# Kernel optimization log

Hardware: AMD Instinct MI355X
Metric: run time of the kernel (lower is better)

## Reference

```python
import jax, jax.numpy as jnp
import numpy as np

# Model dims
E, K, D, F = 8, 2, 1024, 2048   # num_experts, top_k, d_model, d_ff
B, S = 2, 1024                  # batch, seq -> T = 2048 tokens


def setup_inputs() -> dict:
    key = jax.random.key(0)
    k1, k2, k3, k4 = jax.random.split(key, 4)
    hidden = jax.random.normal(k1, (B, S, D), dtype=jnp.float32)
    gate_logits = jax.random.normal(k2, (B * S, E), dtype=jnp.float32)
    # Expert FFN params: expert_e(x) = silu(x @ W1[e]) @ W2[e]
    W1 = jax.random.normal(k3, (E, D, F), dtype=jnp.float32) * 0.02
    W2 = jax.random.normal(k4, (E, F, D), dtype=jnp.float32) * 0.02
    return {"hidden": hidden, "gate_logits": gate_logits, "W1": W1, "W2": W2}


def reference(hidden, gate_logits, W1, W2):
    b, s, d = hidden.shape
    x = hidden.reshape(-1, d)                                  # [T, D]
    # Router: softmax -> top-k -> renormalize (gate_logits path of forward)
    probs = jax.nn.softmax(gate_logits, axis=-1)               # [T, E]
    topk_w, topk_idx = jax.lax.top_k(probs, K)                 # [T, K]
    topk_w = topk_w / jnp.sum(topk_w, axis=-1, keepdims=True)
    # Combine weights as a dense [T, E] map (top_k indices are distinct)
    tok_w = jnp.sum(jax.nn.one_hot(topk_idx, E, dtype=topk_w.dtype)
                    * topk_w[..., None], axis=1)               # [T, E]
    # Grouped expert FFN, expressed densely over the expert axis; the
    # combine weights zero out non-selected experts, so the math equals the
    # original gather -> per-expert GEMM -> weighted scatter-combine.
    h = jax.nn.silu(jnp.einsum('td,edf->tef', x, W1))          # [T, E, F]
    y = jnp.einsum('tef,efd->ted', h, W2)                      # [T, E, D]
    out = jnp.einsum('te,ted->td', tok_w, y)                   # [T, D]
    return out.reshape(b, s, d)
```

## Files before the change

### kernel.cpp

```cpp
#include <hip/hip_runtime.h>
#include <hip/hip_bf16.h>

#define E_N 8
#define D_DIM 1024
#define F_DIM 2048
#define T_N 2048
#define NSLOT 4096

typedef unsigned short u16;
typedef unsigned int u32;
typedef unsigned long long u64;
typedef float floatx4 __attribute__((ext_vector_type(4)));
typedef short bf16x8v __attribute__((ext_vector_type(8)));

__device__ __forceinline__ u16 f2bf(float f) {
    union { float f; u32 u; } v; v.f = f;
    u32 r = v.u + 0x7FFFu + ((v.u >> 16) & 1u);
    return (u16)(r >> 16);
}

__device__ __forceinline__ void gll16(const void* g, void* l) {
    __builtin_amdgcn_global_load_lds((const __attribute__((address_space(1))) void*)g,
                                     (__attribute__((address_space(3))) void*)l, 16, 0, 0);
}

__global__ __launch_bounds__(256) void router_kernel(const float* __restrict__ gl,
                                                     int4* __restrict__ tok_meta,
                                                     float* __restrict__ tok_w0,
                                                     int* __restrict__ bcnt) {
    __shared__ int scnt[E_N];
    const int tid = threadIdx.x, b = blockIdx.x;
    if (tid < E_N) scnt[tid] = 0;
    __syncthreads();
    const int t = b * 256 + tid;
    const float4* gp = (const float4*)(gl + (size_t)t * E_N);
    const float4 x0 = gp[0], x1 = gp[1];
    float l[E_N] = {x0.x, x0.y, x0.z, x0.w, x1.x, x1.y, x1.z, x1.w};
    int e0 = 0; float m0 = l[0];
#pragma unroll
    for (int e = 1; e < E_N; ++e) if (l[e] > m0) { m0 = l[e]; e0 = e; }
    int e1 = -1; float m1 = -1e30f;
#pragma unroll
    for (int e = 0; e < E_N; ++e) if (e != e0 && l[e] > m1) { m1 = l[e]; e1 = e; }
    const float p = __expf(m1 - m0);
    const float w0 = 1.0f / (1.0f + p);
    const int r0 = atomicAdd(&scnt[e0], 1);
    const int r1 = atomicAdd(&scnt[e1], 1);
    tok_meta[t] = make_int4(e0, e1, r0, r1);
    tok_w0[t] = w0;
    __syncthreads();
    if (tid < E_N) bcnt[b * E_N + tid] = scnt[tid];
}

__device__ __forceinline__ void cvt_pair(const float* __restrict__ src, u16* __restrict__ dst,
                                         int R, int C, int tr, int tcp, int e, char* LT) {
    const int r0 = tr << 6, c0 = tcp << 7;
    const int t = threadIdx.x;
    const int rowq = t >> 4, col4 = t & 15;
    const float* sp = src + (size_t)e * R * C + (size_t)(r0 + rowq * 4) * C + c0 + col4 * 4;
    float4 v0[4], v1[4];
#pragma unroll
    for (int i = 0; i < 4; ++i) v0[i] = *(const float4*)(sp + (size_t)i * C);
#pragma unroll
    for (int i = 0; i < 4; ++i) v1[i] = *(const float4*)(sp + (size_t)i * C + 64);
    u16* dp = dst + (size_t)e * R * C;

    const float* f0 = (const float*)v0;
#pragma unroll
    for (int j = 0; j < 4; ++j) {
        const int c = col4 * 4 + j;
        u64 pk = (u64)f2bf(f0[0 * 4 + j]) | ((u64)f2bf(f0[1 * 4 + j]) << 16)
               | ((u64)f2bf(f0[2 * 4 + j]) << 32) | ((u64)f2bf(f0[3 * 4 + j]) << 48);
        *(u64*)(LT + c * 144 + ((rowq ^ col4) << 3)) = pk;
    }
    __syncthreads();
#pragma unroll
    for (int i = 0; i < 2; ++i) {
        const int id = i * 256 + t;
        const int c = id >> 3, seg = id & 7;
        const int x = (c >> 2) & 15;
        u64 q[2];
        q[0] = *(const u64*)(LT + c * 144 + (((2 * seg) ^ x) << 3));
        q[1] = *(const u64*)(LT + c * 144 + (((2 * seg + 1) ^ x) << 3));
        *(uint4*)(dp + (size_t)(c0 + c) * R + r0 + seg * 8) = *(const uint4*)q;
    }
    const float* f1 = (const float*)v1;
#pragma unroll
    for (int j = 0; j < 4; ++j) {
        const int c = col4 * 4 + j;
        u64 pk = (u64)f2bf(f1[0 * 4 + j]) | ((u64)f2bf(f1[1 * 4 + j]) << 16)
               | ((u64)f2bf(f1[2 * 4 + j]) << 32) | ((u64)f2bf(f1[3 * 4 + j]) << 48);
        *(u64*)(LT + 9216 + c * 144 + ((rowq ^ col4) << 3)) = pk;
    }
    __syncthreads();
#pragma unroll
    for (int i = 0; i < 2; ++i) {
        const int id = i * 256 + t;
        const int c = id >> 3, seg = id & 7;
        const int x = (c >> 2) & 15;
        u64 q[2];
        q[0] = *(const u64*)(LT + 9216 + c * 144 + (((2 * seg) ^ x) << 3));
        q[1] = *(const u64*)(LT + 9216 + c * 144 + (((2 * seg + 1) ^ x) << 3));
        *(uint4*)(dp + (size_t)(c0 + 64 + c) * R + r0 + seg * 8) = *(const uint4*)q;
    }
}

__global__ __launch_bounds__(256) void prep_kernel(
        const float* __restrict__ W1, const float* __restrict__ W2,
        const float* __restrict__ X, float* __restrict__ out,
        const int4* __restrict__ tok_meta, const float* __restrict__ tok_w0,
        const int* __restrict__ bcnt,
        int* __restrict__ cnt, int* __restrict__ basep,
        int* __restrict__ slot_tok, float* __restrict__ slot_w,
        u16* __restrict__ W1T, u16* __restrict__ W2T, u16* __restrict__ Xg) {
    __shared__ __align__(16) char LT[18432];
    __shared__ int sb[64];
    const int b = blockIdx.x;
    const int tid = threadIdx.x;
    if (b < 2048) {
        const int e = b >> 8, p = b & 255;
        cvt_pair(W1, W1T, D_DIM, F_DIM, p >> 4, p & 15, e, LT);
    } else if (b < 4096) {
        const int b2 = b - 2048;
        const int e = b2 >> 8, p = b2 & 255;
        cvt_pair(W2, W2T, F_DIM, D_DIM, p >> 3, p & 7, e, LT);
    } else if (b < 4608) {
        const int g = b - 4096;
        if (tid < 64) sb[tid] = bcnt[tid];
        __syncthreads();
        int cntE[E_N], baseE[E_N];
        {
            int s = 0;
#pragma unroll
            for (int e = 0; e < E_N; ++e) {
                int c = 0;
#pragma unroll
                for (int k = 0; k < 8; ++k) c += sb[k * E_N + e];
                cntE[e] = c; baseE[e] = s; s += c;
            }
        }
        const int t = g * 4 + (tid >> 6), lane = tid & 63;
        const int4 mt = tok_meta[t];
        const float w0 = tok_w0[t];
        const int bt = t >> 8;
        int o0 = baseE[mt.x], o1 = baseE[mt.y];
        for (int k = 0; k < bt; ++k) { o0 += sb[k * E_N + mt.x]; o1 += sb[k * E_N + mt.y]; }
        const int s0 = o0 + mt.z, s1 = o1 + mt.w;
        const float* xp = X + (size_t)t * D_DIM + lane * 4;
        u16* g0 = Xg + (size_t)s0 * D_DIM + lane * 4;
        u16* g1 = Xg + (size_t)s1 * D_DIM + lane * 4;
#pragma unroll
        for (int p = 0; p < 4; ++p) {
            const float4 v = *(const float4*)(xp + p * 256);
            union { u16 o[4]; uint2 q; } u;
            u.o[0] = f2bf(v.x); u.o[1] = f2bf(v.y); u.o[2] = f2bf(v.z); u.o[3] = f2bf(v.w);
            *(uint2*)(g0 + p * 256) = u.q;
            *(uint2*)(g1 + p * 256) = u.q;
        }
        if (lane == 0) {
            slot_tok[s0] = t; slot_tok[s1] = t;
            slot_w[s0] = w0; slot_w[s1] = 1.0f - w0;
        }
        if (g == 0 && tid < E_N) { cnt[tid] = cntE[tid]; basep[tid] = baseE[tid]; }
    } else {
        const int z = b - 4608;
        float4 zq = {0.f, 0.f, 0.f, 0.f};
        float* op = out + (size_t)z * 2048 + tid * 8;
        *(float4*)op = zq;
        *(float4*)(op + 4) = zq;
    }
}

template<bool G1>
__global__ __launch_bounds__(256) void moe_gemm_kernel(
        const u16* __restrict__ A, const u16* __restrict__ B,
        const int* __restrict__ cnt, const int* __restrict__ basep,
        const int* __restrict__ slot_tok, const float* __restrict__ slot_w,
        u16* __restrict__ hout, float* __restrict__ out) {
    constexpr int KA = G1 ? D_DIM : F_DIM;
    constexpr int KB = KA;
    constexpr int KIT = 16;
    const int e  = G1 ? blockIdx.z : (blockIdx.z >> 1);
    const int kh = G1 ? 0 : (blockIdx.z & 1);
    const int mt = blockIdx.y;
    const int nt = blockIdx.x;
    const int cnt_e = cnt[e];
    if (mt * 128 >= cnt_e) return;
    const int m0 = basep[e] + mt * 128;
    const int vm = cnt_e - mt * 128;

    __shared__ __align__(16) u16 Alds[8192];
    __shared__ __align__(16) u16 Blds[8192];

    const int tid = threadIdx.x;
    const int wid = tid >> 6, lane = tid & 63;
    const int l3 = lane >> 3, l7 = lane & 7;
    const int stgRow = wid * 8 + l3;
    const int stgCol = ((l7 ^ l3) << 3);

    const u16* aS = A + (size_t)(m0 + stgRow) * KA + kh * (F_DIM / 2) + stgCol;
    const u16* bS = B + (size_t)e * ((size_t)D_DIM * F_DIM)
                      + (size_t)(nt * 128 + stgRow) * KB + kh * (F_DIM / 2) + stgCol;

    const int wm = (wid >> 1) * 64, wn = (wid & 1) * 64;
    const int lr = lane & 15, lq = lane >> 4;
    const int aoff = (wm + lr) * 64;
    const int boff = (wn + lr) * 64;
    const int sw0 = ((lq)     ^ l7) << 3;
    const int sw1 = ((lq + 4) ^ l7) << 3;

    floatx4 acc[4][4];
    const floatx4 zero = {0.f, 0.f, 0.f, 0.f};
#pragma unroll
    for (int i = 0; i < 4; ++i)
#pragma unroll
        for (int j = 0; j < 4; ++j) acc[i][j] = zero;

    for (int kt = 0; kt < KIT; ++kt) {
#pragma unroll
        for (int c = 0; c < 4; ++c) {
            gll16(aS + (size_t)(c * 32) * KA, &Alds[c * 2048 + wid * 512]);
            gll16(bS + (size_t)(c * 32) * KB, &Blds[c * 2048 + wid * 512]);
        }
        aS += 64; bS += 64;
        __syncthreads();
#pragma unroll
        for (int ks = 0; ks < 2; ++ks) {
            const int sw = ks ? sw1 : sw0;
            bf16x8v af[4], bfv[4];
#pragma unroll
            for (int mi = 0; mi < 4; ++mi) af[mi]  = *(const bf16x8v*)&Alds[aoff + mi * 1024 + sw];
#pragma unroll
            for (int ni = 0; ni < 4; ++ni) bfv[ni] = *(const bf16x8v*)&Blds[boff + ni * 1024 + sw];
#pragma unroll
            for (int mi = 0; mi < 4; ++mi)
#pragma unroll
                for (int ni = 0; ni < 4; ++ni)
                    acc[mi][ni] = __builtin_amdgcn_mfma_f32_16x16x32_bf16(af[mi], bfv[ni], acc[mi][ni], 0, 0, 0);
        }
        __syncthreads();
    }

    if constexpr (G1) {
#pragma unroll
        for (int mi = 0; mi < 4; ++mi)
#pragma unroll
            for (int r = 0; r < 4; ++r) {
                const int rl = wm + mi * 16 + lq * 4 + r;
                if (rl < vm) {
                    const float w = slot_w[m0 + rl];
                    u16* hp = hout + (size_t)(m0 + rl) * F_DIM + nt * 128 + wn + lr;
#pragma unroll
                    for (int ni = 0; ni < 4; ++ni) {
                        const float v = acc[mi][ni][r];
                        hp[ni * 16] = f2bf(w * v / (1.0f + __expf(-v)));
                    }
                }
            }
    } else {
#pragma unroll
        for (int mi = 0; mi < 4; ++mi)
#pragma unroll
            for (int r = 0; r < 4; ++r) {
                const int rl = wm + mi * 16 + lq * 4 + r;
                if (rl < vm) {
                    const int tok = slot_tok[m0 + rl];
                    float* op = out + (size_t)tok * D_DIM + nt * 128 + wn + lr;
#pragma unroll
                    for (int ni = 0; ni < 4; ++ni) atomicAdd(&op[ni * 16], acc[mi][ni][r]);
                }
            }
    }
}

extern "C" void kernel_launch(void* const* d_in, const int* in_sizes, int n_in,
                              void* d_out, int out_size, void* d_ws, size_t ws_size,
                              hipStream_t stream) {
    const float* hidden = (const float*)d_in[0];
    const float* gl     = (const float*)d_in[1];
    const float* W1     = (const float*)d_in[2];
    const float* W2     = (const float*)d_in[3];
    float* out = (float*)d_out;

    char* ws = (char*)d_ws;
    int*   cnt      = (int*)(ws + 0);
    int*   basep    = (int*)(ws + 64);
    int*   bcnt     = (int*)(ws + 128);
    int4*  tok_meta = (int4*)(ws + 512);
    float* tok_w0   = (float*)(ws + 512 + 32768);
    int*   slot_tok = (int*)(ws + 512 + 40960);
    float* slot_w   = (float*)(ws + 512 + 57344);

    const size_t META    = 131072;
    const size_t HBYTES  = (size_t)(NSLOT + 128) * F_DIM * 2;
    const size_t W1BYTES = (size_t)E_N * D_DIM * F_DIM * 2;
    const size_t XBYTES  = (size_t)(NSLOT + 128) * D_DIM * 2;
    u16* h   = (u16*)(ws + META);
    u16* W1T = (u16*)(ws + META + HBYTES);
    u16* Xg  = (u16*)(ws + META + HBYTES + W1BYTES);
    u16* W2T = (u16*)(ws + META + HBYTES + W1BYTES + XBYTES);

    router_kernel<<<8, 256, 0, stream>>>(gl, tok_meta, tok_w0, bcnt);
    prep_kernel<<<5632, 256, 0, stream>>>(W1, W2, hidden, out, tok_meta, tok_w0, bcnt,
                                          cnt, basep, slot_tok, slot_w, W1T, W2T, Xg);
    moe_gemm_kernel<true><<<dim3(F_DIM / 128, 16, E_N), 256, 0, stream>>>(
        Xg, W1T, cnt, basep, slot_tok, slot_w, h, nullptr);
    moe_gemm_kernel<false><<<dim3(D_DIM / 128, 16, E_N * 2), 256, 0, stream>>>(
        h, W2T, cnt, basep, slot_tok, slot_w, nullptr, out);
}
```

Baseline: 258.9 us.

## Fuse fp32-to-bf16 weight and activation conversion into MoE GEMM tile loads

Removes the separate prep pass that transposed and converted W1/W2 to bf16 and gathered X into a bf16 buffer. The GEMM kernels now read fp32 weights and gathered token rows directly, convert them with v_cvt_pk_bf16_f32 and store them into swizzled LDS. The second GEMM drops its K-split. The aim is to avoid writing and re-reading bf16 copies of the weights, but every expert tile now re-reads and re-converts fp32 weights, using synchronous scalar-strided loads instead of async global-to-LDS loads, which gives up load/compute overlap.

```diff
diff --git a/kernel.cpp b/kernel.cpp
--- a/kernel.cpp
+++ b/kernel.cpp
@@ -13,10 +13,10 @@
 typedef float floatx4 __attribute__((ext_vector_type(4)));
 typedef short bf16x8v __attribute__((ext_vector_type(8)));
 
-__device__ __forceinline__ u16 f2bf(float f) {
-    union { float f; u32 u; } v; v.f = f;
-    u32 r = v.u + 0x7FFFu + ((v.u >> 16) & 1u);
-    return (u16)(r >> 16);
+__device__ __forceinline__ u32 cvtpk(float a, float b) {
+    u32 r;
+    asm("v_cvt_pk_bf16_f32 %0, %1, %2" : "=v"(r) : "v"(a), "v"(b));
+    return r;
 }
 
 __device__ __forceinline__ void gll16(const void* g, void* l) {
@@ -52,138 +52,58 @@
     if (tid < E_N) bcnt[b * E_N + tid] = scnt[tid];
 }
 
-__device__ __forceinline__ void cvt_pair(const float* __restrict__ src, u16* __restrict__ dst,
-                                         int R, int C, int tr, int tcp, int e, char* LT) {
-    const int r0 = tr << 6, c0 = tcp << 7;
-    const int t = threadIdx.x;
-    const int rowq = t >> 4, col4 = t & 15;
-    const float* sp = src + (size_t)e * R * C + (size_t)(r0 + rowq * 4) * C + c0 + col4 * 4;
-    float4 v0[4], v1[4];
-#pragma unroll
-    for (int i = 0; i < 4; ++i) v0[i] = *(const float4*)(sp + (size_t)i * C);
-#pragma unroll
-    for (int i = 0; i < 4; ++i) v1[i] = *(const float4*)(sp + (size_t)i * C + 64);
-    u16* dp = dst + (size_t)e * R * C;
-
-    const float* f0 = (const float*)v0;
-#pragma unroll
-    for (int j = 0; j < 4; ++j) {
-        const int c = col4 * 4 + j;
-        u64 pk = (u64)f2bf(f0[0 * 4 + j]) | ((u64)f2bf(f0[1 * 4 + j]) << 16)
-               | ((u64)f2bf(f0[2 * 4 + j]) << 32) | ((u64)f2bf(f0[3 * 4 + j]) << 48);
-        *(u64*)(LT + c * 144 + ((rowq ^ col4) << 3)) = pk;
-    }
-    __syncthreads();
-#pragma unroll
-    for (int i = 0; i < 2; ++i) {
-        const int id = i * 256 + t;
-        const int c = id >> 3, seg = id & 7;
-        const int x = (c >> 2) & 15;
-        u64 q[2];
-        q[0] = *(const u64*)(LT + c * 144 + (((2 * seg) ^ x) << 3));
-        q[1] = *(const u64*)(LT + c * 144 + (((2 * seg + 1) ^ x) << 3));
-        *(uint4*)(dp + (size_t)(c0 + c) * R + r0 + seg * 8) = *(const uint4*)q;
-    }
-    const float* f1 = (const float*)v1;
-#pragma unroll
-    for (int j = 0; j < 4; ++j) {
-        const int c = col4 * 4 + j;
-        u64 pk = (u64)f2bf(f1[0 * 4 + j]) | ((u64)f2bf(f1[1 * 4 + j]) << 16)
-               | ((u64)f2bf(f1[2 * 4 + j]) << 32) | ((u64)f2bf(f1[3 * 4 + j]) << 48);
-        *(u64*)(LT + 9216 + c * 144 + ((rowq ^ col4) << 3)) = pk;
-    }
-    __syncthreads();
-#pragma unroll
-    for (int i = 0; i < 2; ++i) {
-        const int id = i * 256 + t;
-        const int c = id >> 3, seg = id & 7;
-        const int x = (c >> 2) & 15;
-        u64 q[2];
-        q[0] = *(const u64*)(LT + 9216 + c * 144 + (((2 * seg) ^ x) << 3));
-        q[1] = *(const u64*)(LT + 9216 + c * 144 + (((2 * seg + 1) ^ x) << 3));
-        *(uint4*)(dp + (size_t)(c0 + 64 + c) * R + r0 + seg * 8) = *(const uint4*)q;
-    }
-}
-
-__global__ __launch_bounds__(256) void prep_kernel(
-        const float* __restrict__ W1, const float* __restrict__ W2,
-        const float* __restrict__ X, float* __restrict__ out,
+__global__ __launch_bounds__(256) void finalize_kernel(
         const int4* __restrict__ tok_meta, const float* __restrict__ tok_w0,
         const int* __restrict__ bcnt,
         int* __restrict__ cnt, int* __restrict__ basep,
         int* __restrict__ slot_tok, float* __restrict__ slot_w,
-        u16* __restrict__ W1T, u16* __restrict__ W2T, u16* __restrict__ Xg) {
-    __shared__ __align__(16) char LT[18432];
-    __shared__ int sb[64];
-    const int b = blockIdx.x;
-    const int tid = threadIdx.x;
-    if (b < 2048) {
-        const int e = b >> 8, p = b & 255;
-        cvt_pair(W1, W1T, D_DIM, F_DIM, p >> 4, p & 15, e, LT);
-    } else if (b < 4096) {
-        const int b2 = b - 2048;
-        const int e = b2 >> 8, p = b2 & 255;
-        cvt_pair(W2, W2T, F_DIM, D_DIM, p >> 3, p & 7, e, LT);
-    } else if (b < 4608) {
-        const int g = b - 4096;
+        float* __restrict__ out) {
+    const int b = blockIdx.x, tid = threadIdx.x;
+    if (b < 8) {
+        __shared__ int sb[64];
         if (tid < 64) sb[tid] = bcnt[tid];
         __syncthreads();
         int cntE[E_N], baseE[E_N];
-        {
-            int s = 0;
-#pragma unroll
-            for (int e = 0; e < E_N; ++e) {
-                int c = 0;
-#pragma unroll
-                for (int k = 0; k < 8; ++k) c += sb[k * E_N + e];
-                cntE[e] = c; baseE[e] = s; s += c;
-            }
-        }
-        const int t = g * 4 + (tid >> 6), lane = tid & 63;
+        int s = 0;
+#pragma unroll
+        for (int e = 0; e < E_N; ++e) {
+            int c = 0;
+#pragma unroll
+            for (int k = 0; k < 8; ++k) c += sb[k * E_N + e];
+            cntE[e] = c; baseE[e] = s; s += c;
+        }
+        const int t = b * 256 + tid;
         const int4 mt = tok_meta[t];
+        int o0 = baseE[mt.x], o1 = baseE[mt.y];
+        for (int k = 0; k < b; ++k) { o0 += sb[k * E_N + mt.x]; o1 += sb[k * E_N + mt.y]; }
+        const int s0 = o0 + mt.z, s1 = o1 + mt.w;
         const float w0 = tok_w0[t];
-        const int bt = t >> 8;
-        int o0 = baseE[mt.x], o1 = baseE[mt.y];
-        for (int k = 0; k < bt; ++k) { o0 += sb[k * E_N + mt.x]; o1 += sb[k * E_N + mt.y]; }
-        const int s0 = o0 + mt.z, s1 = o1 + mt.w;
-        const float* xp = X + (size_t)t * D_DIM + lane * 4;
-        u16* g0 = Xg + (size_t)s0 * D_DIM + lane * 4;
-        u16* g1 = Xg + (size_t)s1 * D_DIM + lane * 4;
-#pragma unroll
-        for (int p = 0; p < 4; ++p) {
-            const float4 v = *(const float4*)(xp + p * 256);
-            union { u16 o[4]; uint2 q; } u;
-            u.o[0] = f2bf(v.x); u.o[1] = f2bf(v.y); u.o[2] = f2bf(v.z); u.o[3] = f2bf(v.w);
-            *(uint2*)(g0 + p * 256) = u.q;
-            *(uint2*)(g1 + p * 256) = u.q;
-        }
-        if (lane == 0) {
-            slot_tok[s0] = t; slot_tok[s1] = t;
-            slot_w[s0] = w0; slot_w[s1] = 1.0f - w0;
-        }
-        if (g == 0 && tid < E_N) { cnt[tid] = cntE[tid]; basep[tid] = baseE[tid]; }
+        slot_tok[s0] = t; slot_tok[s1] = t;
+        slot_w[s0] = w0; slot_w[s1] = 1.0f - w0;
+        if (b == 0 && tid < E_N) { cnt[tid] = cntE[tid]; basep[tid] = baseE[tid]; }
+        if (b == 0) slot_tok[NSLOT + tid] = 0;
     } else {
-        const int z = b - 4608;
-        float4 zq = {0.f, 0.f, 0.f, 0.f};
-        float* op = out + (size_t)z * 2048 + tid * 8;
-        *(float4*)op = zq;
-        *(float4*)(op + 4) = zq;
+        const int z = b - 8;
+        const float4 zq = {0.f, 0.f, 0.f, 0.f};
+        float* op = out + (size_t)z * 4096 + tid * 16;
+        *(float4*)op = zq; *(float4*)(op + 4) = zq;
+        *(float4*)(op + 8) = zq; *(float4*)(op + 12) = zq;
     }
 }
 
 template<bool G1>
-__global__ __launch_bounds__(256) void moe_gemm_kernel(
-        const u16* __restrict__ A, const u16* __restrict__ B,
+__global__ __launch_bounds__(256, 3) void moe_gemm_kernel(
+        const float* __restrict__ Xf, const u16* __restrict__ Ah,
+        const float* __restrict__ Wf,
         const int* __restrict__ cnt, const int* __restrict__ basep,
         const int* __restrict__ slot_tok, const float* __restrict__ slot_w,
         u16* __restrict__ hout, float* __restrict__ out) {
-    constexpr int KA = G1 ? D_DIM : F_DIM;
-    constexpr int KB = KA;
-    constexpr int KIT = 16;
-    const int e  = G1 ? blockIdx.z : (blockIdx.z >> 1);
-    const int kh = G1 ? 0 : (blockIdx.z & 1);
-    const int mt = blockIdx.y;
-    const int nt = blockIdx.x;
+    constexpr int KDIM = G1 ? D_DIM : F_DIM;
+    constexpr int NDIM = G1 ? F_DIM : D_DIM;
+    constexpr int KIT  = KDIM / 64;
+    const int mt = blockIdx.x;
+    const int nt = blockIdx.y;
+    const int e  = blockIdx.z;
     const int cnt_e = cnt[e];
     if (mt * 128 >= cnt_e) return;
     const int m0 = basep[e] + mt * 128;
@@ -194,19 +114,26 @@
 
     const int tid = threadIdx.x;
     const int wid = tid >> 6, lane = tid & 63;
-    const int l3 = lane >> 3, l7 = lane & 7;
-    const int stgRow = wid * 8 + l3;
-    const int stgCol = ((l7 ^ l3) << 3);
-
-    const u16* aS = A + (size_t)(m0 + stgRow) * KA + kh * (F_DIM / 2) + stgCol;
-    const u16* bS = B + (size_t)e * ((size_t)D_DIM * F_DIM)
-                      + (size_t)(nt * 128 + stgRow) * KB + kh * (F_DIM / 2) + stgCol;
+
+    const float* aF = nullptr; const u16* aH = nullptr;
+    const int awm = tid >> 1, awk = (tid & 1) * 4;
+    if constexpr (G1) {
+        const int tok = slot_tok[m0 + awm];
+        aF = Xf + (size_t)tok * D_DIM + (tid & 1) * 32;
+    } else {
+        const int l3 = lane >> 3, l7 = lane & 7;
+        aH = Ah + (size_t)(m0 + wid * 8 + l3) * KDIM + ((l7 ^ l3) << 3);
+    }
+
+    const int n_loc = tid & 127;
+    const int bh = __builtin_amdgcn_readfirstlane(tid >> 7);
+    const float* bBase = Wf + (size_t)e * KDIM * NDIM + (size_t)(bh * 32) * NDIM + nt * 128;
 
     const int wm = (wid >> 1) * 64, wn = (wid & 1) * 64;
-    const int lr = lane & 15, lq = lane >> 4;
+    const int lr = lane & 15, lq = lane >> 4, l7 = lane & 7;
     const int aoff = (wm + lr) * 64;
     const int boff = (wn + lr) * 64;
-    const int sw0 = ((lq)     ^ l7) << 3;
+    const int sw0 = (lq ^ l7) << 3;
     const int sw1 = ((lq + 4) ^ l7) << 3;
 
     floatx4 acc[4][4];
@@ -217,12 +144,45 @@
         for (int j = 0; j < 4; ++j) acc[i][j] = zero;
 
     for (int kt = 0; kt < KIT; ++kt) {
-#pragma unroll
-        for (int c = 0; c < 4; ++c) {
-            gll16(aS + (size_t)(c * 32) * KA, &Alds[c * 2048 + wid * 512]);
-            gll16(bS + (size_t)(c * 32) * KB, &Blds[c * 2048 + wid * 512]);
-        }
-        aS += 64; bS += 64;
+        if constexpr (G1) {
+            float4 av[8];
+#pragma unroll
+            for (int i = 0; i < 8; ++i) av[i] = *(const float4*)(aF + i * 4);
+            aF += 64;
+            const float* f = (const float*)av;
+#pragma unroll
+            for (int c = 0; c < 4; ++c) {
+                const u32 w0 = cvtpk(f[c * 8 + 0], f[c * 8 + 1]);
+                const u32 w1 = cvtpk(f[c * 8 + 2], f[c * 8 + 3]);
+                const u32 w2 = cvtpk(f[c * 8 + 4], f[c * 8 + 5]);
+                const u32 w3 = cvtpk(f[c * 8 + 6], f[c * 8 + 7]);
+                const int s = awk + c;
+                *(uint4*)((char*)Alds + awm * 128 + ((s ^ (awm & 7)) << 4)) =
+                    make_uint4(w0, w1, w2, w3);
+            }
+        } else {
+#pragma unroll
+            for (int c = 0; c < 4; ++c)
+                gll16(aH + (size_t)(c * 32) * KDIM, (char*)Alds + c * 4096 + wid * 1024);
+            aH += 64;
+        }
+        {
+            const size_t krow = (size_t)kt * 64 * NDIM;
+#pragma unroll
+            for (int q = 0; q < 4; ++q) {
+                float v[8];
+#pragma unroll
+                for (int j = 0; j < 8; ++j)
+                    v[j] = bBase[krow + (size_t)(q * 8 + j) * NDIM + n_loc];
+                const u32 w0 = cvtpk(v[0], v[1]);
+                const u32 w1 = cvtpk(v[2], v[3]);
+                const u32 w2 = cvtpk(v[4], v[5]);
+                const u32 w3 = cvtpk(v[6], v[7]);
+                const int s = bh * 4 + q;
+                *(uint4*)((char*)Blds + n_loc * 128 + ((s ^ (n_loc & 7)) << 4)) =
+                    make_uint4(w0, w1, w2, w3);
+            }
+        }
         __syncthreads();
 #pragma unroll
         for (int ks = 0; ks < 2; ++ks) {
@@ -253,7 +213,9 @@
 #pragma unroll
                     for (int ni = 0; ni < 4; ++ni) {
                         const float v = acc[mi][ni][r];
-                        hp[ni * 16] = f2bf(w * v / (1.0f + __expf(-v)));
+                        union { float f; u32 u; } cv; cv.f = w * v / (1.0f + __expf(-v));
+                        const u32 rr = cv.u + 0x7FFFu + ((cv.u >> 16) & 1u);
+                        hp[ni * 16] = (u16)(rr >> 16);
                     }
                 }
             }
@@ -287,24 +249,17 @@
     int*   basep    = (int*)(ws + 64);
     int*   bcnt     = (int*)(ws + 128);
     int4*  tok_meta = (int4*)(ws + 512);
-    float* tok_w0   = (float*)(ws + 512 + 32768);
-    int*   slot_tok = (int*)(ws + 512 + 40960);
-    float* slot_w   = (float*)(ws + 512 + 57344);
-
-    const size_t META    = 131072;
-    const size_t HBYTES  = (size_t)(NSLOT + 128) * F_DIM * 2;
-    const size_t W1BYTES = (size_t)E_N * D_DIM * F_DIM * 2;
-    const size_t XBYTES  = (size_t)(NSLOT + 128) * D_DIM * 2;
-    u16* h   = (u16*)(ws + META);
-    u16* W1T = (u16*)(ws + META + HBYTES);
-    u16* Xg  = (u16*)(ws + META + HBYTES + W1BYTES);
-    u16* W2T = (u16*)(ws + META + HBYTES + W1BYTES + XBYTES);
+    float* tok_w0   = (float*)(ws + 33280);
+    int*   slot_tok = (int*)(ws + 41472);
+    float* slot_w   = (float*)(ws + 58880);
+
+    u16* h = (u16*)(ws + 131072);
 
     router_kernel<<<8, 256, 0, stream>>>(gl, tok_meta, tok_w0, bcnt);
-    prep_kernel<<<5632, 256, 0, stream>>>(W1, W2, hidden, out, tok_meta, tok_w0, bcnt,
-                                          cnt, basep, slot_tok, slot_w, W1T, W2T, Xg);
-    moe_gemm_kernel<true><<<dim3(F_DIM / 128, 16, E_N), 256, 0, stream>>>(
-        Xg, W1T, cnt, basep, slot_tok, slot_w, h, nullptr);
-    moe_gemm_kernel<false><<<dim3(D_DIM / 128, 16, E_N * 2), 256, 0, stream>>>(
-        h, W2T, cnt, basep, slot_tok, slot_w, nullptr, out);
-}
+    finalize_kernel<<<520, 256, 0, stream>>>(tok_meta, tok_w0, bcnt,
+                                             cnt, basep, slot_tok, slot_w, out);
+    moe_gemm_kernel<true><<<dim3(16, F_DIM / 128, E_N), 256, 0, stream>>>(
+        hidden, nullptr, W1, cnt, basep, slot_tok, slot_w, h, nullptr);
+    moe_gemm_kernel<false><<<dim3(16, D_DIM / 128, E_N), 256, 0, stream>>>(
+        nullptr, h, W2, cnt, basep, slot_tok, slot_w, nullptr, out);
+}
```

After: 657.5 us. 2.54x slower.
